# Kernel optimization log

Hardware: AMD Instinct MI355X
Metric: run time of the kernel (lower is better)

## Reference

```python
import jax, jax.numpy as jnp
import numpy as np

EPS = 1e-5  # torch group_norm default
GROUPS = 32


def _nin(t, W, b):
    # torch Nin: einsum('bchw,co->bowh') transposes spatial dims, then adds bias
    return jnp.einsum('bchw,co->bowh', t, W) + b


def setup_inputs() -> dict:
    key = jax.random.key(0)
    ks = jax.random.split(key, 9)
    B, C, N = 16, 512, 32
    x = jax.random.normal(ks[0], (B, C, N, N), jnp.float32)
    sc = 0.02
    Wq = jax.random.normal(ks[1], (C, C), jnp.float32) * sc
    Wk = jax.random.normal(ks[2], (C, C), jnp.float32) * sc
    Wv = jax.random.normal(ks[3], (C, C), jnp.float32) * sc
    Wn = jax.random.normal(ks[4], (C, C), jnp.float32) * sc
    bq = jnp.zeros((1, C, 1, 1), jnp.float32)
    bk = jnp.zeros((1, C, 1, 1), jnp.float32)
    bv = jnp.zeros((1, C, 1, 1), jnp.float32)
    bn = jnp.zeros((1, C, 1, 1), jnp.float32)
    return {"x": x, "Wq": Wq, "bq": bq, "Wk": Wk, "bk": bk,
            "Wv": Wv, "bv": bv, "Wn": Wn, "bn": bn}


def reference(x, Wq, bq, Wk, bk, Wv, bv, Wn, bn):
    B, C, H, W = x.shape
    # GroupNorm(32) with no affine params
    xg = x.reshape(B, GROUPS, -1)
    mu = xg.mean(-1, keepdims=True)
    var = xg.var(-1, keepdims=True)
    h = ((xg - mu) / jnp.sqrt(var + EPS)).reshape(B, C, H, W)
    # Nin projections -> spatially transposed (B, C, W, H)
    q = _nin(h, Wq, bq)
    k = _nin(h, Wk, bk)
    v = _nin(h, Wv, bv)
    # scores s[b,w1,w2,h1,h2] = sum_c q[b,c,w1,h1] k[b,c,w2,h2] * C^-0.5
    s = jnp.einsum('bcwh,bcWH->bwWhH', q, k) * (C ** -0.5)
    # softmax over flat (h1,h2) blocks exactly as the torch reshape does
    s = jax.nn.softmax(s.reshape(B, H, W, H * W), axis=-1).reshape(B, H, W, H, W)
    # torch.einsum('bHWHW, bcWH -> bcWH', w, v) takes the DIAGONAL over the
    # repeated H and W labels: diag[b,i,j] = s[b,i,j,i,j], then elementwise
    # scales v: out[b,c,w,h] = diag[b,h,w] * v[b,c,w,h]
    i = jnp.arange(H)
    j = jnp.arange(W)
    diag = s[:, i[:, None], j[None, :], i[:, None], j[None, :]]  # (B,H,W)
    h2 = v * jnp.swapaxes(diag, 1, 2)[:, None]  # (B,C,W,H)
    out = _nin(h2, Wn, bn)  # transposes back -> (B,C,H,W)
    return x + out
```

## Files before the change

### kernel.cpp

```cpp
#include <hip/hip_runtime.h>
#include <hip/hip_bf16.h>

typedef __attribute__((ext_vector_type(8))) short short8;
typedef __attribute__((ext_vector_type(4))) float floatx4;

#define MFMA16(a, b, c) __builtin_amdgcn_mfma_f32_16x16x32_bf16((a), (b), (c), 0, 0, 0)

__device__ __forceinline__ short f2bf(float f) {
    union { float f; unsigned u; } x; x.f = f;
    unsigned r = (x.u + 0x7fffu + ((x.u >> 16) & 1u)) >> 16;
    return (short)r;
}

__device__ __forceinline__ void gl2lds16(const short* g, short* l) {
    void* gv = const_cast<short*>(g);
    __builtin_amdgcn_global_load_lds((__attribute__((address_space(1))) void*)gv,
                                     (__attribute__((address_space(3))) void*)l,
                                     16, 0, 0);
}

__global__ void transpose_w4(const float* __restrict__ Wq, const float* __restrict__ Wk,
                             const float* __restrict__ Wv, const float* __restrict__ Wn,
                             const float* __restrict__ bq, const float* __restrict__ bk,
                             const float* __restrict__ bv,
                             short* __restrict__ Wqkv_t, short* __restrict__ Wn_t,
                             float* __restrict__ bias_cat) {
    __shared__ float t[32][33];
    int z = blockIdx.z;
    const float* Wsrc = (z == 0) ? Wq : (z == 1) ? Wk : (z == 2) ? Wv : Wn;
    int o0 = blockIdx.x * 32, c0 = blockIdx.y * 32;
    int lx = threadIdx.x, ly = threadIdx.y;
    for (int i = ly; i < 32; i += 8) t[i][lx] = Wsrc[(size_t)(c0 + i) * 512 + o0 + lx];
    __syncthreads();
    for (int i = ly; i < 32; i += 8) {
        short v = f2bf(t[lx][i]);
        if (z < 3) Wqkv_t[(size_t)(z * 512 + o0 + i) * 512 + c0 + lx] = v;
        else       Wn_t[(size_t)(o0 + i) * 512 + c0 + lx] = v;
    }
    if (z < 3 && blockIdx.y == 0 && ly == 0) {
        const float* bsrc = (z == 0) ? bq : (z == 1) ? bk : bv;
        bias_cat[z * 512 + o0 + lx] = bsrc[o0 + lx];
    }
}

__global__ __launch_bounds__(256) void groupnorm_k(const float* __restrict__ x,
                                                   short* __restrict__ hnt) {
    int b = blockIdx.x >> 5, g = blockIdx.x & 31;
    const float* xg = x + ((size_t)b * 512 + g * 16) * 1024;
    const float4* xg4 = (const float4*)xg;
    float s = 0.f, ss = 0.f;
    for (int i = threadIdx.x; i < 4096; i += 256) {
        float4 v = xg4[i];
        s  += v.x + v.y + v.z + v.w;
        ss += v.x * v.x + v.y * v.y + v.z * v.z + v.w * v.w;
    }
#pragma unroll
    for (int off = 32; off > 0; off >>= 1) {
        s  += __shfl_down(s,  off, 64);
        ss += __shfl_down(ss, off, 64);
    }
    __shared__ float red[8];
    int w = threadIdx.x >> 6;
    if ((threadIdx.x & 63) == 0) { red[w] = s; red[4 + w] = ss; }
    __syncthreads();
    float S  = red[0] + red[1] + red[2] + red[3];
    float SS = red[4] + red[5] + red[6] + red[7];
    float mean = S * (1.f / 16384.f);
    float var  = SS * (1.f / 16384.f) - mean * mean;
    float rstd = rsqrtf(var + 1e-5f);
    __shared__ __attribute__((aligned(16))) short tile[16 * 1026];
    for (int i = threadIdx.x; i < 4096; i += 256) {
        float4 v = xg4[i];
        int c = i >> 8, p = (i & 255) * 4;
        short* tp = tile + c * 1026 + p;
        tp[0] = f2bf((v.x - mean) * rstd);
        tp[1] = f2bf((v.y - mean) * rstd);
        tp[2] = f2bf((v.z - mean) * rstd);
        tp[3] = f2bf((v.w - mean) * rstd);
    }
    __syncthreads();
    for (int i = threadIdx.x; i < 2048; i += 256) {
        int p = i >> 1, half = i & 1;
        short8 v;
#pragma unroll
        for (int j = 0; j < 8; ++j) v[j] = tile[(half * 8 + j) * 1026 + p];
        *(short8*)(hnt + ((size_t)b * 1024 + p) * 512 + g * 16 + half * 8) = v;
    }
}

__global__ __launch_bounds__(256) void qkv_gemm(const short* __restrict__ A,
                                                const short* __restrict__ Wt,
                                                const float* __restrict__ bias_cat,
                                                short* __restrict__ Qp,
                                                short* __restrict__ Kp,
                                                short* __restrict__ Vb) {
    const int tid = threadIdx.x;
    const int wv = tid >> 6, ln = tid & 63;
    const int m0 = blockIdx.x * 128, n0 = blockIdx.y * 128;
    const size_t BS = 1024 * 512;
    const short* Ab = A + (size_t)blockIdx.z * BS;
    const int tsel = n0 >> 9;
    const int permute = (tsel < 2);
    short* Ob = ((tsel == 0) ? Qp : (tsel == 1) ? Kp : Vb) + (size_t)blockIdx.z * BS;

    __shared__ __attribute__((aligned(16))) short As[128 * 32];
    __shared__ __attribute__((aligned(16))) short Bs[128 * 32];

    floatx4 acc[4][4] = {};
    const int wm = (wv >> 1) * 64, wn = (wv & 1) * 64;
    const int fr = ln & 15, fq = ln >> 4;

    for (int kk = 0; kk < 512; kk += 32) {
        __syncthreads();
#pragma unroll
        for (int j = 0; j < 2; ++j) {
            int s = (wv * 2 + j) * 64 + ln;
            int r = s >> 2;
            int q = (s & 3) ^ ((r >> 1) & 3);
            gl2lds16(Ab + (size_t)(m0 + r) * 512 + kk + q * 8, As + (size_t)(wv * 2 + j) * 512);
            gl2lds16(Wt + (size_t)(n0 + r) * 512 + kk + q * 8, Bs + (size_t)(wv * 2 + j) * 512);
        }
        __syncthreads();
        short8 af[4], bfr[4];
#pragma unroll
        for (int t = 0; t < 4; ++t) {
            int ra = wm + t * 16 + fr;
            af[t]  = *(const short8*)(As + ra * 32 + ((fq ^ ((ra >> 1) & 3)) * 8));
            int rb = wn + t * 16 + fr;
            bfr[t] = *(const short8*)(Bs + rb * 32 + ((fq ^ ((rb >> 1) & 3)) * 8));
        }
#pragma unroll
        for (int mt = 0; mt < 4; ++mt)
#pragma unroll
            for (int nt = 0; nt < 4; ++nt)
                acc[mt][nt] = MFMA16(af[mt], bfr[nt], acc[mt][nt]);
    }
#pragma unroll
    for (int mt = 0; mt < 4; ++mt) {
#pragma unroll
        for (int nt = 0; nt < 4; ++nt) {
            int n = n0 + wn + nt * 16 + fr;
            float bvv = bias_cat[n];
            int nn = n & 511;
#pragma unroll
            for (int r = 0; r < 4; ++r) {
                int m = m0 + wm + mt * 16 + fq * 4 + r;
                int mrow = permute ? ((m & 31) * 32 + (m >> 5)) : m;
                Ob[(size_t)mrow * 512 + nn] = f2bf(acc[mt][nt][r] + bvv);
            }
        }
    }
}

__global__ __launch_bounds__(256, 2) void attn_sm(const short* __restrict__ Qp,
                                                  const short* __restrict__ Kp,
                                                  float* __restrict__ Dm) {
    const int tid = threadIdx.x;
    const int wv = tid >> 6, ln = tid & 63;
    const int m0 = blockIdx.x * 128, n0 = blockIdx.y * 256, b = blockIdx.z;
    const short* Qb = Qp + (size_t)b * (1024 * 512);
    const short* Kb = Kp + (size_t)b * (1024 * 512);

    __shared__ __attribute__((aligned(16))) short As[128 * 32];
    __shared__ __attribute__((aligned(16))) short Bs[256 * 32];

    floatx4 acc[4][8] = {};
    const int wm = (wv >> 1) * 64, wn = (wv & 1) * 128;
    const int fr = ln & 15, fq = ln >> 4;

    for (int kk = 0; kk < 512; kk += 32) {
        __syncthreads();
#pragma unroll
        for (int j = 0; j < 2; ++j) {
            int s = (wv * 2 + j) * 64 + ln;
            int r = s >> 2;
            int q = (s & 3) ^ ((r >> 1) & 3);
            gl2lds16(Qb + (size_t)(m0 + r) * 512 + kk + q * 8, As + (size_t)(wv * 2 + j) * 512);
        }
#pragma unroll
        for (int j = 0; j < 4; ++j) {
            int s = (wv * 4 + j) * 64 + ln;
            int r = s >> 2;
            int q = (s & 3) ^ ((r >> 1) & 3);
            gl2lds16(Kb + (size_t)(n0 + r) * 512 + kk + q * 8, Bs + (size_t)(wv * 4 + j) * 512);
        }
        __syncthreads();
        short8 af[4], bfr[8];
#pragma unroll
        for (int t = 0; t < 4; ++t) {
            int ra = wm + t * 16 + fr;
            af[t] = *(const short8*)(As + ra * 32 + ((fq ^ ((ra >> 1) & 3)) * 8));
        }
#pragma unroll
        for (int u = 0; u < 8; ++u) {
            int rb = wn + u * 16 + fr;
            bfr[u] = *(const short8*)(Bs + rb * 32 + ((fq ^ ((rb >> 1) & 3)) * 8));
        }
#pragma unroll
        for (int mt = 0; mt < 4; ++mt)
#pragma unroll
            for (int nt = 0; nt < 8; ++nt)
                acc[mt][nt] = MFMA16(af[mt], bfr[nt], acc[mt][nt]);
    }

    const float scale = 0.04419417382415922f;
    const int wbase = (m0 + wm) >> 5;
    const int Wbase = (n0 + wn) >> 5;
#pragma unroll
    for (int si = 0; si < 2; ++si) {
#pragma unroll
        for (int sj = 0; sj < 4; ++sj) {
            int wg = wbase + si, Wg = Wbase + sj;
            float tv[16];
            float mx = -3.0e38f;
#pragma unroll
            for (int mi = 0; mi < 2; ++mi)
#pragma unroll
                for (int ni = 0; ni < 2; ++ni)
#pragma unroll
                    for (int r = 0; r < 4; ++r) {
                        float u = acc[2 * si + mi][2 * sj + ni][r] * scale;
                        tv[(mi * 2 + ni) * 4 + r] = u;
                        mx = fmaxf(mx, u);
                    }
#pragma unroll
            for (int off = 32; off > 0; off >>= 1) mx = fmaxf(mx, __shfl_xor(mx, off, 64));
            float se = 0.f;
#pragma unroll
            for (int i = 0; i < 16; ++i) se += __expf(tv[i] - mx);
#pragma unroll
            for (int off = 32; off > 0; off >>= 1) se += __shfl_xor(se, off, 64);
            if (fq == ((wg >> 2) & 3) && fr == (Wg & 15)) {
                int mi = wg >> 4, ni = Wg >> 4;
                float numer = tv[(mi * 2 + ni) * 4 + (wg & 3)];
                Dm[((size_t)b * 32 + wg) * 32 + Wg] = __expf(numer - mx) / se;
            }
        }
    }
}

__global__ __launch_bounds__(256) void out_gemm(const short* __restrict__ A,
                                                const short* __restrict__ Wt,
                                                const float* __restrict__ Dm,
                                                const float* __restrict__ bnb,
                                                const float* __restrict__ x,
                                                float* __restrict__ out) {
    const int tid = threadIdx.x;
    const int wv = tid >> 6, ln = tid & 63;
    const int m0 = blockIdx.x * 128, n0 = blockIdx.y * 128, b = blockIdx.z;
    const size_t BS = 1024 * 512;
    const short* Ab = A + (size_t)b * BS;

    __shared__ __attribute__((aligned(16))) short As[128 * 32];
    __shared__ __attribute__((aligned(16))) short Bs[128 * 32];

    floatx4 acc[4][4] = {};
    const int wm = (wv >> 1) * 64, wn = (wv & 1) * 64;
    const int fr = ln & 15, fq = ln >> 4;

    for (int kk = 0; kk < 512; kk += 32) {
        __syncthreads();
#pragma unroll
        for (int j = 0; j < 2; ++j) {
            int s = (wv * 2 + j) * 64 + ln;
            int r = s >> 2;
            int q = (s & 3) ^ ((r >> 1) & 3);
            gl2lds16(Ab + (size_t)(m0 + r) * 512 + kk + q * 8, As + (size_t)(wv * 2 + j) * 512);
            gl2lds16(Wt + (size_t)(n0 + r) * 512 + kk + q * 8, Bs + (size_t)(wv * 2 + j) * 512);
        }
        __syncthreads();
        short8 af[4], bfr[4];
#pragma unroll
        for (int t = 0; t < 4; ++t) {
            int ra = wm + t * 16 + fr;
            af[t]  = *(const short8*)(As + ra * 32 + ((fq ^ ((ra >> 1) & 3)) * 8));
            int rb = wn + t * 16 + fr;
            bfr[t] = *(const short8*)(Bs + rb * 32 + ((fq ^ ((rb >> 1) & 3)) * 8));
        }
#pragma unroll
        for (int mt = 0; mt < 4; ++mt)
#pragma unroll
            for (int nt = 0; nt < 4; ++nt)
                acc[mt][nt] = MFMA16(af[mt], bfr[nt], acc[mt][nt]);
    }
#pragma unroll
    for (int mt = 0; mt < 4; ++mt) {
        int mbase = m0 + wm + mt * 16 + fq * 4;
        float4 d4 = *(const float4*)(Dm + (size_t)b * 1024 + mbase);
#pragma unroll
        for (int nt = 0; nt < 4; ++nt) {
            int n = n0 + wn + nt * 16 + fr;
            float bvv = bnb[n];
            size_t base = ((size_t)b * 512 + n) * 1024 + mbase;
            float4 x4 = *(const float4*)(x + base);
            float4 o;
            o.x = x4.x + d4.x * acc[mt][nt][0] + bvv;
            o.y = x4.y + d4.y * acc[mt][nt][1] + bvv;
            o.z = x4.z + d4.z * acc[mt][nt][2] + bvv;
            o.w = x4.w + d4.w * acc[mt][nt][3] + bvv;
            *(float4*)(out + base) = o;
        }
    }
}

extern "C" void kernel_launch(void* const* d_in, const int* in_sizes, int n_in,
                              void* d_out, int out_size, void* d_ws, size_t ws_size,
                              hipStream_t stream) {
    const float* x  = (const float*)d_in[0];
    const float* Wq = (const float*)d_in[1];
    const float* bq = (const float*)d_in[2];
    const float* Wk = (const float*)d_in[3];
    const float* bk = (const float*)d_in[4];
    const float* Wv = (const float*)d_in[5];
    const float* bv = (const float*)d_in[6];
    const float* Wn = (const float*)d_in[7];
    const float* bn = (const float*)d_in[8];
    float* out = (float*)d_out;
    char* ws = (char*)d_ws;

    const size_t WQKV = (size_t)1536 * 512 * 2;
    const size_t WSZ  = (size_t)512 * 512 * 2;
    const size_t BIAS = 1536 * sizeof(float);
    const size_t TSZ  = (size_t)16 * 1024 * 512 * 2;
    short* Wqkv_t   = (short*)(ws);
    short* Wn_t     = (short*)(ws + WQKV);
    float* bias_cat = (float*)(ws + WQKV + WSZ);
    char*  base     = ws + WQKV + WSZ + BIAS;
    short* hnt = (short*)(base);
    short* Qp  = (short*)(base + TSZ);
    short* Kp  = (short*)(base + 2 * TSZ);
    short* Vb  = (short*)(base + 3 * TSZ);
    float* Dm  = (float*)(base + 4 * TSZ);

    transpose_w4<<<dim3(16, 16, 4), dim3(32, 8), 0, stream>>>(
        Wq, Wk, Wv, Wn, bq, bk, bv, Wqkv_t, Wn_t, bias_cat);
    groupnorm_k<<<512, 256, 0, stream>>>(x, hnt);
    qkv_gemm<<<dim3(8, 12, 16), 256, 0, stream>>>(hnt, Wqkv_t, bias_cat, Qp, Kp, Vb);
    attn_sm<<<dim3(8, 4, 16), 256, 0, stream>>>(Qp, Kp, Dm);
    out_gemm<<<dim3(8, 4, 16), 256, 0, stream>>>(Vb, Wn_t, Dm, bn, x, out);
}
```

Before: 213.0 us.

## Fold Wq·Wk^T into one weight and drop the separate Q and K projections

The scores q·k are rewritten as h·(Wq Wk^T)·h plus bias cross terms. A small GEMM builds the combined 512x512 weight, and one GEMM now computes T = h·M together with V, replacing the three Q/K/V projections. The attention GEMM then reads T and the normalized h directly through a permuted row index. Bias terms are added as per-row and per-column vectors (gemv) plus a constant. This saves one large projection GEMM and its write, but adds small prep kernels and rounds the fused weight to bf16, which changes numerics slightly. The V GEMM tile is also enlarged to 256 rows.

After: 222.9 us. 1.05x slower.

```diff
diff --git a/kernel.cpp b/kernel.cpp
--- a/kernel.cpp
+++ b/kernel.cpp
@@ -10,6 +10,10 @@
     union { float f; unsigned u; } x; x.f = f;
     unsigned r = (x.u + 0x7fffu + ((x.u >> 16) & 1u)) >> 16;
     return (short)r;
+}
+__device__ __forceinline__ float bf2f(short s) {
+    union { float f; unsigned u; } x; x.u = ((unsigned)(unsigned short)s) << 16;
+    return x.f;
 }
 
 __device__ __forceinline__ void gl2lds16(const short* g, short* l) {
@@ -19,28 +23,100 @@
                                      16, 0, 0);
 }
 
-__global__ void transpose_w4(const float* __restrict__ Wq, const float* __restrict__ Wk,
-                             const float* __restrict__ Wv, const float* __restrict__ Wn,
-                             const float* __restrict__ bq, const float* __restrict__ bk,
-                             const float* __restrict__ bv,
-                             short* __restrict__ Wqkv_t, short* __restrict__ Wn_t,
-                             float* __restrict__ bias_cat) {
+__global__ void prep_w(const float* __restrict__ Wq, const float* __restrict__ Wk,
+                       const float* __restrict__ Wv, const float* __restrict__ Wn,
+                       short* __restrict__ wqb, short* __restrict__ wkb,
+                       short* __restrict__ Wtv, short* __restrict__ Wn_t) {
     __shared__ float t[32][33];
     int z = blockIdx.z;
-    const float* Wsrc = (z == 0) ? Wq : (z == 1) ? Wk : (z == 2) ? Wv : Wn;
     int o0 = blockIdx.x * 32, c0 = blockIdx.y * 32;
     int lx = threadIdx.x, ly = threadIdx.y;
-    for (int i = ly; i < 32; i += 8) t[i][lx] = Wsrc[(size_t)(c0 + i) * 512 + o0 + lx];
-    __syncthreads();
-    for (int i = ly; i < 32; i += 8) {
-        short v = f2bf(t[lx][i]);
-        if (z < 3) Wqkv_t[(size_t)(z * 512 + o0 + i) * 512 + c0 + lx] = v;
-        else       Wn_t[(size_t)(o0 + i) * 512 + c0 + lx] = v;
-    }
-    if (z < 3 && blockIdx.y == 0 && ly == 0) {
-        const float* bsrc = (z == 0) ? bq : (z == 1) ? bk : bv;
-        bias_cat[z * 512 + o0 + lx] = bsrc[o0 + lx];
-    }
+    if (z < 2) {
+        const float* src = z ? Wk : Wq;
+        short* dst = z ? wkb : wqb;
+        for (int i = ly; i < 32; i += 8)
+            dst[(size_t)(c0 + i) * 512 + o0 + lx] = f2bf(src[(size_t)(c0 + i) * 512 + o0 + lx]);
+    } else {
+        const float* src = (z == 2) ? Wv : Wn;
+        short* dst = (z == 2) ? (Wtv + (size_t)512 * 512) : Wn_t;
+        for (int i = ly; i < 32; i += 8) t[i][lx] = src[(size_t)(c0 + i) * 512 + o0 + lx];
+        __syncthreads();
+        for (int i = ly; i < 32; i += 8) dst[(size_t)(o0 + i) * 512 + c0 + lx] = f2bf(t[lx][i]);
+    }
+}
+
+__global__ void prep_vec(const float* __restrict__ Wq, const float* __restrict__ Wk,
+                         const float* __restrict__ bq, const float* __restrict__ bk,
+                         float* __restrict__ wu, float* __restrict__ wv2,
+                         float* __restrict__ cstp) {
+    int c = blockIdx.x, ln = threadIdx.x;
+    float su = 0.f, sv = 0.f;
+    for (int o = ln; o < 512; o += 64) {
+        su += Wq[(size_t)c * 512 + o] * bk[o];
+        sv += Wk[(size_t)c * 512 + o] * bq[o];
+    }
+#pragma unroll
+    for (int off = 32; off > 0; off >>= 1) {
+        su += __shfl_down(su, off, 64);
+        sv += __shfl_down(sv, off, 64);
+    }
+    if (ln == 0) { wu[c] = su; wv2[c] = sv; }
+    if (c == 0) {
+        float sc = 0.f;
+        for (int o = ln; o < 512; o += 64) sc += bq[o] * bk[o];
+#pragma unroll
+        for (int off = 32; off > 0; off >>= 1) sc += __shfl_down(sc, off, 64);
+        if (ln == 0) cstp[0] = sc;
+    }
+}
+
+__global__ __launch_bounds__(256) void g_gemm(const short* __restrict__ A,
+                                              const short* __restrict__ B,
+                                              short* __restrict__ Out) {
+    const int tid = threadIdx.x;
+    const int wv = tid >> 6, ln = tid & 63;
+    const int m0 = blockIdx.x * 128, n0 = blockIdx.y * 128;
+    __shared__ __attribute__((aligned(16))) short As[128 * 32];
+    __shared__ __attribute__((aligned(16))) short Bs[128 * 32];
+    floatx4 acc[4][4] = {};
+    const int wm = (wv >> 1) * 64, wn = (wv & 1) * 64;
+    const int fr = ln & 15, fq = ln >> 4;
+    for (int kk = 0; kk < 512; kk += 32) {
+        __syncthreads();
+#pragma unroll
+        for (int j = 0; j < 2; ++j) {
+            int s = (wv * 2 + j) * 64 + ln;
+            int r = s >> 2;
+            int q = (s & 3) ^ ((r >> 1) & 3);
+            gl2lds16(A + (size_t)(m0 + r) * 512 + kk + q * 8, As + (size_t)(wv * 2 + j) * 512);
+            gl2lds16(B + (size_t)(n0 + r) * 512 + kk + q * 8, Bs + (size_t)(wv * 2 + j) * 512);
+        }
+        __syncthreads();
+        short8 af[4], bfr[4];
+#pragma unroll
+        for (int t = 0; t < 4; ++t) {
+            int ra = wm + t * 16 + fr;
+            af[t]  = *(const short8*)(As + ra * 32 + ((fq ^ ((ra >> 1) & 3)) * 8));
+            int rb = wn + t * 16 + fr;
+            bfr[t] = *(const short8*)(Bs + rb * 32 + ((fq ^ ((rb >> 1) & 3)) * 8));
+        }
+#pragma unroll
+        for (int mt = 0; mt < 4; ++mt)
+#pragma unroll
+            for (int nt = 0; nt < 4; ++nt)
+                acc[mt][nt] = MFMA16(af[mt], bfr[nt], acc[mt][nt]);
+    }
+#pragma unroll
+    for (int mt = 0; mt < 4; ++mt)
+#pragma unroll
+        for (int nt = 0; nt < 4; ++nt) {
+            int n = n0 + wn + nt * 16 + fr;
+#pragma unroll
+            for (int r = 0; r < 4; ++r) {
+                int m = m0 + wm + mt * 16 + fq * 4 + r;
+                Out[(size_t)m * 512 + n] = f2bf(acc[mt][nt][r]);
+            }
+        }
 }
 
 __global__ __launch_bounds__(256) void groupnorm_k(const float* __restrict__ x,
@@ -88,78 +164,117 @@
     }
 }
 
-__global__ __launch_bounds__(256) void qkv_gemm(const short* __restrict__ A,
-                                                const short* __restrict__ Wt,
-                                                const float* __restrict__ bias_cat,
-                                                short* __restrict__ Qp,
-                                                short* __restrict__ Kp,
-                                                short* __restrict__ Vb) {
+__global__ __launch_bounds__(256) void uv_gemv(const short* __restrict__ hnt,
+                                               const float* __restrict__ wu,
+                                               const float* __restrict__ wv2,
+                                               float* __restrict__ u1p,
+                                               float* __restrict__ v2p) {
+    __shared__ float wus[512], wvs[512];
+    for (int i = threadIdx.x; i < 512; i += 256) { wus[i] = wu[i]; wvs[i] = wv2[i]; }
+    __syncthreads();
+    int wv_ = threadIdx.x >> 6, ln = threadIdx.x & 63;
+    int row = blockIdx.x * 4 + wv_;
+    int b = row >> 10, p = row & 1023;
+    short8 h = *(const short8*)(hnt + (size_t)row * 512 + ln * 8);
+    float su = 0.f, sv = 0.f;
+#pragma unroll
+    for (int j = 0; j < 8; ++j) {
+        float hv = bf2f(h[j]);
+        su += hv * wus[ln * 8 + j];
+        sv += hv * wvs[ln * 8 + j];
+    }
+#pragma unroll
+    for (int off = 32; off > 0; off >>= 1) {
+        su += __shfl_down(su, off, 64);
+        sv += __shfl_down(sv, off, 64);
+    }
+    if (ln == 0) {
+        int pp = ((p & 31) << 5) | (p >> 5);
+        u1p[b * 1024 + pp] = su;
+        v2p[b * 1024 + pp] = sv;
+    }
+}
+
+__global__ __launch_bounds__(256, 2) void tv_gemm(const short* __restrict__ A,
+                                                  const short* __restrict__ Wt,
+                                                  const float* __restrict__ bv,
+                                                  short* __restrict__ T,
+                                                  short* __restrict__ Vb) {
     const int tid = threadIdx.x;
     const int wv = tid >> 6, ln = tid & 63;
-    const int m0 = blockIdx.x * 128, n0 = blockIdx.y * 128;
+    const int m0 = blockIdx.x * 256, n0 = blockIdx.y * 128;
     const size_t BS = 1024 * 512;
     const short* Ab = A + (size_t)blockIdx.z * BS;
     const int tsel = n0 >> 9;
-    const int permute = (tsel < 2);
-    short* Ob = ((tsel == 0) ? Qp : (tsel == 1) ? Kp : Vb) + (size_t)blockIdx.z * BS;
-
-    __shared__ __attribute__((aligned(16))) short As[128 * 32];
+    short* Ob = (tsel ? Vb : T) + (size_t)blockIdx.z * BS;
+
+    __shared__ __attribute__((aligned(16))) short As[256 * 32];
     __shared__ __attribute__((aligned(16))) short Bs[128 * 32];
 
-    floatx4 acc[4][4] = {};
-    const int wm = (wv >> 1) * 64, wn = (wv & 1) * 64;
+    floatx4 acc[8][4] = {};
+    const int wm = (wv >> 1) * 128, wn = (wv & 1) * 64;
     const int fr = ln & 15, fq = ln >> 4;
 
     for (int kk = 0; kk < 512; kk += 32) {
         __syncthreads();
+#pragma unroll
+        for (int j = 0; j < 4; ++j) {
+            int s = (wv * 4 + j) * 64 + ln;
+            int r = s >> 2;
+            int q = (s & 3) ^ ((r >> 1) & 3);
+            gl2lds16(Ab + (size_t)(m0 + r) * 512 + kk + q * 8, As + (size_t)(wv * 4 + j) * 512);
+        }
 #pragma unroll
         for (int j = 0; j < 2; ++j) {
             int s = (wv * 2 + j) * 64 + ln;
             int r = s >> 2;
             int q = (s & 3) ^ ((r >> 1) & 3);
-            gl2lds16(Ab + (size_t)(m0 + r) * 512 + kk + q * 8, As + (size_t)(wv * 2 + j) * 512);
             gl2lds16(Wt + (size_t)(n0 + r) * 512 + kk + q * 8, Bs + (size_t)(wv * 2 + j) * 512);
         }
         __syncthreads();
-        short8 af[4], bfr[4];
-#pragma unroll
-        for (int t = 0; t < 4; ++t) {
+        short8 af[8], bfr[4];
+#pragma unroll
+        for (int t = 0; t < 8; ++t) {
             int ra = wm + t * 16 + fr;
-            af[t]  = *(const short8*)(As + ra * 32 + ((fq ^ ((ra >> 1) & 3)) * 8));
-            int rb = wn + t * 16 + fr;
-            bfr[t] = *(const short8*)(Bs + rb * 32 + ((fq ^ ((rb >> 1) & 3)) * 8));
-        }
-#pragma unroll
-        for (int mt = 0; mt < 4; ++mt)
+            af[t] = *(const short8*)(As + ra * 32 + ((fq ^ ((ra >> 1) & 3)) * 8));
+        }
+#pragma unroll
+        for (int u = 0; u < 4; ++u) {
+            int rb = wn + u * 16 + fr;
+            bfr[u] = *(const short8*)(Bs + rb * 32 + ((fq ^ ((rb >> 1) & 3)) * 8));
+        }
+#pragma unroll
+        for (int mt = 0; mt < 8; ++mt)
 #pragma unroll
             for (int nt = 0; nt < 4; ++nt)
                 acc[mt][nt] = MFMA16(af[mt], bfr[nt], acc[mt][nt]);
     }
 #pragma unroll
-    for (int mt = 0; mt < 4; ++mt) {
+    for (int mt = 0; mt < 8; ++mt)
 #pragma unroll
         for (int nt = 0; nt < 4; ++nt) {
             int n = n0 + wn + nt * 16 + fr;
-            float bvv = bias_cat[n];
+            float bvv = tsel ? bv[n - 512] : 0.0f;
             int nn = n & 511;
 #pragma unroll
             for (int r = 0; r < 4; ++r) {
                 int m = m0 + wm + mt * 16 + fq * 4 + r;
-                int mrow = permute ? ((m & 31) * 32 + (m >> 5)) : m;
-                Ob[(size_t)mrow * 512 + nn] = f2bf(acc[mt][nt][r] + bvv);
+                Ob[(size_t)m * 512 + nn] = f2bf(acc[mt][nt][r] + bvv);
             }
         }
-    }
-}
-
-__global__ __launch_bounds__(256, 2) void attn_sm(const short* __restrict__ Qp,
-                                                  const short* __restrict__ Kp,
+}
+
+__global__ __launch_bounds__(256, 2) void attn_sm(const short* __restrict__ Tt,
+                                                  const short* __restrict__ Hn,
+                                                  const float* __restrict__ u1p,
+                                                  const float* __restrict__ v2p,
+                                                  const float* __restrict__ cstp,
                                                   float* __restrict__ Dm) {
     const int tid = threadIdx.x;
     const int wv = tid >> 6, ln = tid & 63;
     const int m0 = blockIdx.x * 128, n0 = blockIdx.y * 256, b = blockIdx.z;
-    const short* Qb = Qp + (size_t)b * (1024 * 512);
-    const short* Kb = Kp + (size_t)b * (1024 * 512);
+    const short* Tb = Tt + (size_t)b * (1024 * 512);
+    const short* Hb = Hn + (size_t)b * (1024 * 512);
 
     __shared__ __attribute__((aligned(16))) short As[128 * 32];
     __shared__ __attribute__((aligned(16))) short Bs[256 * 32];
@@ -168,22 +283,34 @@
     const int wm = (wv >> 1) * 64, wn = (wv & 1) * 128;
     const int fr = ln & 15, fq = ln >> 4;
 
+    size_t offA[2], offB[4];
+#pragma unroll
+    for (int j = 0; j < 2; ++j) {
+        int s = (wv * 2 + j) * 64 + ln;
+        int r = s >> 2;
+        int q = (s & 3) ^ ((r >> 1) & 3);
+        int m = m0 + r;
+        int pm = ((m & 31) << 5) | (m >> 5);
+        offA[j] = (size_t)pm * 512 + q * 8;
+    }
+#pragma unroll
+    for (int j = 0; j < 4; ++j) {
+        int s = (wv * 4 + j) * 64 + ln;
+        int r = s >> 2;
+        int q = (s & 3) ^ ((r >> 1) & 3);
+        int m = n0 + r;
+        int pm = ((m & 31) << 5) | (m >> 5);
+        offB[j] = (size_t)pm * 512 + q * 8;
+    }
+
     for (int kk = 0; kk < 512; kk += 32) {
         __syncthreads();
 #pragma unroll
-        for (int j = 0; j < 2; ++j) {
-            int s = (wv * 2 + j) * 64 + ln;
-            int r = s >> 2;
-            int q = (s & 3) ^ ((r >> 1) & 3);
-            gl2lds16(Qb + (size_t)(m0 + r) * 512 + kk + q * 8, As + (size_t)(wv * 2 + j) * 512);
-        }
-#pragma unroll
-        for (int j = 0; j < 4; ++j) {
-            int s = (wv * 4 + j) * 64 + ln;
-            int r = s >> 2;
-            int q = (s & 3) ^ ((r >> 1) & 3);
-            gl2lds16(Kb + (size_t)(n0 + r) * 512 + kk + q * 8, Bs + (size_t)(wv * 4 + j) * 512);
-        }
+        for (int j = 0; j < 2; ++j)
+            gl2lds16(Tb + offA[j] + kk, As + (size_t)(wv * 2 + j) * 512);
+#pragma unroll
+        for (int j = 0; j < 4; ++j)
+            gl2lds16(Hb + offB[j] + kk, Bs + (size_t)(wv * 4 + j) * 512);
         __syncthreads();
         short8 af[4], bfr[8];
 #pragma unroll
@@ -204,6 +331,7 @@
     }
 
     const float scale = 0.04419417382415922f;
+    const float cst = cstp[0];
     const int wbase = (m0 + wm) >> 5;
     const int Wbase = (n0 + wn) >> 5;
 #pragma unroll
@@ -216,13 +344,16 @@
 #pragma unroll
             for (int mi = 0; mi < 2; ++mi)
 #pragma unroll
-                for (int ni = 0; ni < 2; ++ni)
+                for (int ni = 0; ni < 2; ++ni) {
+                    float vc = v2p[b * 1024 + Wg * 32 + ni * 16 + fr];
 #pragma unroll
                     for (int r = 0; r < 4; ++r) {
-                        float u = acc[2 * si + mi][2 * sj + ni][r] * scale;
+                        float uc = u1p[b * 1024 + wg * 32 + mi * 16 + fq * 4 + r];
+                        float u = (acc[2 * si + mi][2 * sj + ni][r] + uc + vc + cst) * scale;
                         tv[(mi * 2 + ni) * 4 + r] = u;
                         mx = fmaxf(mx, u);
                     }
+                }
 #pragma unroll
             for (int off = 32; off > 0; off >>= 1) mx = fmaxf(mx, __shfl_xor(mx, off, 64));
             float se = 0.f;
@@ -318,24 +449,29 @@
     float* out = (float*)d_out;
     char* ws = (char*)d_ws;
 
-    const size_t WQKV = (size_t)1536 * 512 * 2;
-    const size_t WSZ  = (size_t)512 * 512 * 2;
-    const size_t BIAS = 1536 * sizeof(float);
-    const size_t TSZ  = (size_t)16 * 1024 * 512 * 2;
-    short* Wqkv_t   = (short*)(ws);
-    short* Wn_t     = (short*)(ws + WQKV);
-    float* bias_cat = (float*)(ws + WQKV + WSZ);
-    char*  base     = ws + WQKV + WSZ + BIAS;
+    const size_t WSZ = (size_t)512 * 512 * 2;
+    const size_t TSZ = (size_t)16 * 1024 * 512 * 2;
+    short* wqb  = (short*)(ws);
+    short* wkb  = (short*)(ws + WSZ);
+    short* Wtv  = (short*)(ws + 2 * WSZ);
+    short* Wn_t = (short*)(ws + 4 * WSZ);
+    float* wu   = (float*)(ws + 5 * WSZ);
+    float* wv2  = (float*)(ws + 5 * WSZ + 2048);
+    float* cstp = (float*)(ws + 5 * WSZ + 4096);
+    char*  base = ws + 5 * WSZ + 8192;
     short* hnt = (short*)(base);
-    short* Qp  = (short*)(base + TSZ);
-    short* Kp  = (short*)(base + 2 * TSZ);
-    short* Vb  = (short*)(base + 3 * TSZ);
-    float* Dm  = (float*)(base + 4 * TSZ);
-
-    transpose_w4<<<dim3(16, 16, 4), dim3(32, 8), 0, stream>>>(
-        Wq, Wk, Wv, Wn, bq, bk, bv, Wqkv_t, Wn_t, bias_cat);
+    short* T   = (short*)(base + TSZ);
+    short* Vb  = (short*)(base + 2 * TSZ);
+    float* u1p = (float*)(base + 3 * TSZ);
+    float* v2p = (float*)(base + 3 * TSZ + 65536);
+    float* Dm  = (float*)(base + 3 * TSZ + 131072);
+
+    prep_w<<<dim3(16, 16, 4), dim3(32, 8), 0, stream>>>(Wq, Wk, Wv, Wn, wqb, wkb, Wtv, Wn_t);
+    g_gemm<<<dim3(4, 4, 1), 256, 0, stream>>>(wkb, wqb, Wtv);
+    prep_vec<<<512, 64, 0, stream>>>(Wq, Wk, bq, bk, wu, wv2, cstp);
     groupnorm_k<<<512, 256, 0, stream>>>(x, hnt);
-    qkv_gemm<<<dim3(8, 12, 16), 256, 0, stream>>>(hnt, Wqkv_t, bias_cat, Qp, Kp, Vb);
-    attn_sm<<<dim3(8, 4, 16), 256, 0, stream>>>(Qp, Kp, Dm);
+    uv_gemv<<<4096, 256, 0, stream>>>(hnt, wu, wv2, u1p, v2p);
+    tv_gemm<<<dim3(4, 8, 16), 256, 0, stream>>>(hnt, Wtv, bv, T, Vb);
+    attn_sm<<<dim3(8, 4, 16), 256, 0, stream>>>(T, hnt, u1p, v2p, cstp, Dm);
     out_gemm<<<dim3(8, 4, 16), 256, 0, stream>>>(Vb, Wn_t, Dm, bn, x, out);
 }
```
